# Performance work log

Measured on AMD Instinct MI355X. Metric: run time of the kernel, lower is better.

The kernel has to match this reference:

```python
import jax, jax.numpy as jnp
import numpy as np

MODEL_DIM = 1024
RANK = 128

def setup_inputs() -> dict:
    key = jax.random.key(0)
    k1, k2 = jax.random.split(key)
    batch = jax.random.normal(k1, (8, 512, MODEL_DIM), dtype=jnp.float32)
    # nn.init.uniform_(proj, -0.05, 0.05)
    proj = jax.random.uniform(k2, (MODEL_DIM, RANK), dtype=jnp.float32, minval=-0.05, maxval=0.05)
    return {"batch": batch, "proj": proj}

def reference(batch, proj):
    # project: (B, S, D) @ (D, R) -> (B, S, R)
    transformed = jnp.matmul(batch, proj)
    # all-pairs squared L2 distance via broadcast diff, matching the torch math
    # diffs: (B, S, S, R)
    diffs = transformed[:, :, None, :] - transformed[:, None, :, :]
    squared_distances = jnp.sum(diffs * diffs, axis=-1)  # (B, S, S)
    return squared_distances
```

## Files before the change

### kernel.cpp

```cpp
#include <hip/hip_runtime.h>

#define SEQ 512
#define MD  1024
#define RK  128

typedef __attribute__((ext_vector_type(8))) short  bf16x8;
typedef __attribute__((ext_vector_type(4))) float  floatx4;
typedef __attribute__((ext_vector_type(4))) unsigned int uint4v;
typedef __attribute__((ext_vector_type(4))) unsigned short ushortx4;

__device__ inline unsigned short f2bf(float f) {
    union { float f; unsigned u; } v; v.f = f;
    unsigned r = v.u + 0x7fffu + ((v.u >> 16) & 1u);
    return (unsigned short)(r >> 16);
}

__global__ __launch_bounds__(256) void transpose_proj(
    const float* __restrict__ proj, unsigned short* __restrict__ Pt)
{
    __shared__ float Ls[64 * 68];
    const int t  = threadIdx.x;
    const int k0 = (blockIdx.x >> 1) * 64;
    const int n0 = (blockIdx.x & 1) * 64;

    {
        int kr = t >> 2;
        int nc = (t & 3) * 16;
        #pragma unroll
        for (int c = 0; c < 4; ++c) {
            float4 v = *(const float4*)(proj + (size_t)(k0 + kr) * RK + n0 + nc + c * 4);
            *(float4*)(Ls + kr * 68 + nc + c * 4) = v;
        }
    }
    __syncthreads();
    {
        int nl = t >> 2;
        int kh = (t & 3) * 16;
        unsigned short tmp[16];
        #pragma unroll
        for (int kk = 0; kk < 16; ++kk)
            tmp[kk] = f2bf(Ls[(kh + kk) * 68 + nl]);
        *(uint4v*)(Pt + (size_t)(n0 + nl) * MD + k0 + kh)     = *(uint4v*)(tmp);
        *(uint4v*)(Pt + (size_t)(n0 + nl) * MD + k0 + kh + 8) = *(uint4v*)(tmp + 8);
    }
}

#define REDW 2112

__global__ __launch_bounds__(512) void proj_mfma(
    const float* __restrict__ batch, const unsigned short* __restrict__ Pt,
    unsigned short* __restrict__ T, float* __restrict__ Nrm)
{
    __shared__ float Red[8 * REDW];

    const int t    = threadIdx.x;
    const int w    = t >> 6;
    const int l    = t & 63;
    const int lm   = l & 15;
    const int quad = l >> 4;
    const int r0   = blockIdx.x * 16;

    floatx4 acc[8];
    #pragma unroll
    for (int i = 0; i < 8; ++i) acc[i] = (floatx4){0.f, 0.f, 0.f, 0.f};

    const float* arow = batch + (size_t)(r0 + lm) * MD + w * 128 + quad * 8;

    #pragma unroll
    for (int s = 0; s < 4; ++s) {
        float4 a0 = *(const float4*)(arow + s * 32);
        float4 a1 = *(const float4*)(arow + s * 32 + 4);
        bf16x8 av;
        av[0] = (short)f2bf(a0.x); av[1] = (short)f2bf(a0.y);
        av[2] = (short)f2bf(a0.z); av[3] = (short)f2bf(a0.w);
        av[4] = (short)f2bf(a1.x); av[5] = (short)f2bf(a1.y);
        av[6] = (short)f2bf(a1.z); av[7] = (short)f2bf(a1.w);
        #pragma unroll
        for (int nt = 0; nt < 8; ++nt) {
            bf16x8 bv = *(const bf16x8*)(Pt + (size_t)(nt * 16 + lm) * MD
                                         + w * 128 + s * 32 + quad * 8);
            acc[nt] = __builtin_amdgcn_mfma_f32_16x16x32_bf16(av, bv, acc[nt], 0, 0, 0);
        }
    }

    #pragma unroll
    for (int nt = 0; nt < 8; ++nt) {
        #pragma unroll
        for (int r = 0; r < 4; ++r) {
            Red[w * REDW + (quad * 4 + r) * 132 + nt * 16 + lm] = acc[nt][r];
        }
    }
    __syncthreads();

    {
        const int row  = t >> 5;
        const int col4 = (t & 31) * 4;
        float4 s4 = {0.f, 0.f, 0.f, 0.f};
        #pragma unroll
        for (int ww = 0; ww < 8; ++ww) {
            float4 p = *(const float4*)(Red + ww * REDW + row * 132 + col4);
            s4.x += p.x; s4.y += p.y; s4.z += p.z; s4.w += p.w;
        }
        unsigned short tmp[4];
        tmp[0] = f2bf(s4.x); tmp[1] = f2bf(s4.y);
        tmp[2] = f2bf(s4.z); tmp[3] = f2bf(s4.w);
        *(ushortx4*)(T + (size_t)(r0 + row) * RK + col4) = *(ushortx4*)tmp;

        float ss = s4.x * s4.x + s4.y * s4.y + s4.z * s4.z + s4.w * s4.w;
        ss += __shfl_xor(ss, 1,  64);
        ss += __shfl_xor(ss, 2,  64);
        ss += __shfl_xor(ss, 4,  64);
        ss += __shfl_xor(ss, 8,  64);
        ss += __shfl_xor(ss, 16, 64);
        if ((t & 31) == 0) Nrm[r0 + row] = ss;
    }
}

#define LDB 136

__global__ __launch_bounds__(256) void dist_mfma(
    const unsigned short* __restrict__ T, const float* __restrict__ Nrm,
    float* __restrict__ out)
{
    __shared__ unsigned short Ti[64 * LDB];
    __shared__ unsigned short Tj[64 * LDB];
    __shared__ float nI[64], nJ[64];

    const int t    = threadIdx.x;
    const int w    = t >> 6;
    const int l    = t & 63;
    const int lm   = l & 15;
    const int quad = l >> 4;
    const int jt = blockIdx.x, it = blockIdx.y, b = blockIdx.z;
    const int i0 = it * 64, j0 = jt * 64;
    const unsigned short* Tb = T + (size_t)b * SEQ * RK;

    {
        int row = t >> 2, kq = (t & 3) * 32;
        const unsigned short* si = Tb + (size_t)(i0 + row) * RK + kq;
        const unsigned short* sj = Tb + (size_t)(j0 + row) * RK + kq;
        #pragma unroll
        for (int q = 0; q < 4; ++q) {
            *(uint4v*)(Ti + row * LDB + kq + q * 8) = *(const uint4v*)(si + q * 8);
            *(uint4v*)(Tj + row * LDB + kq + q * 8) = *(const uint4v*)(sj + q * 8);
        }
        if (t < 64)                nI[t]      = Nrm[(size_t)b * SEQ + i0 + t];
        else if (t < 128)          nJ[t - 64] = Nrm[(size_t)b * SEQ + j0 + (t - 64)];
    }
    __syncthreads();

    floatx4 acc[4];
    #pragma unroll
    for (int i = 0; i < 4; ++i) acc[i] = (floatx4){0.f, 0.f, 0.f, 0.f};

    #pragma unroll
    for (int s = 0; s < 4; ++s) {
        bf16x8 av = *(const bf16x8*)(Ti + (w * 16 + lm) * LDB + s * 32 + quad * 8);
        #pragma unroll
        for (int nt = 0; nt < 4; ++nt) {
            bf16x8 bv = *(const bf16x8*)(Tj + (nt * 16 + lm) * LDB + s * 32 + quad * 8);
            acc[nt] = __builtin_amdgcn_mfma_f32_16x16x32_bf16(av, bv, acc[nt], 0, 0, 0);
        }
    }

    float niv[4];
    #pragma unroll
    for (int r = 0; r < 4; ++r) niv[r] = nI[w * 16 + quad * 4 + r];

    float* ob = out + ((size_t)b * SEQ + (i0 + w * 16)) * SEQ + j0;
    #pragma unroll
    for (int nt = 0; nt < 4; ++nt) {
        float njv = nJ[nt * 16 + lm];
        #pragma unroll
        for (int r = 0; r < 4; ++r) {
            ob[(size_t)(quad * 4 + r) * SEQ + nt * 16 + lm] =
                niv[r] + njv - 2.f * acc[nt][r];
        }
    }
}

extern "C" void kernel_launch(void* const* d_in, const int* in_sizes, int n_in,
                              void* d_out, int out_size, void* d_ws, size_t ws_size,
                              hipStream_t stream) {
    const float* batch = (const float*)d_in[0];
    const float* proj  = (const float*)d_in[1];
    float* out = (float*)d_out;

    unsigned short* T   = (unsigned short*)d_ws;
    unsigned short* Pt  = (unsigned short*)((char*)d_ws + (1 << 20));
    float*          Nrm = (float*)((char*)d_ws + (1 << 20) + (1 << 18));

    transpose_proj<<<32, 256, 0, stream>>>(proj, Pt);
    proj_mfma<<<256, 512, 0, stream>>>(batch, Pt, T, Nrm);
    dist_mfma<<<dim3(8, 8, 8), 256, 0, stream>>>(T, Nrm, out);
}
```

Baseline: 79.58 us.

## Fuse transpose, projection and distance kernels into one cooperative launch

Replaces three separate kernel launches with a single cooperative kernel of 512 blocks that uses grid-wide syncs between the proj-transpose, projection GEMM and pairwise-distance phases. The projection phase now uses 256-thread blocks with 4 waves each covering 256 of K, so the shared-memory reduction has 4 partials instead of 8. This is meant to remove inter-kernel launch gaps. In exchange it adds grid.sync overhead and fewer threads in the projection stage, and it depends on all 512 blocks being co-resident.

Result: slower. 210.5 us (+164.5%).

```diff
diff --git a/kernel.cpp b/kernel.cpp
--- a/kernel.cpp
+++ b/kernel.cpp
@@ -1,4 +1,7 @@
 #include <hip/hip_runtime.h>
+#include <hip/hip_cooperative_groups.h>
+
+namespace cg = cooperative_groups;
 
 #define SEQ 512
 #define MD  1024
@@ -15,166 +18,170 @@
     return (unsigned short)(r >> 16);
 }
 
-__global__ __launch_bounds__(256) void transpose_proj(
-    const float* __restrict__ proj, unsigned short* __restrict__ Pt)
+#define LDB  136
+#define REDW 2112
+
+__global__ __launch_bounds__(256, 2) void fused_probe(
+    const float* __restrict__ batch, const float* __restrict__ proj,
+    unsigned short* __restrict__ Pt, unsigned short* __restrict__ T,
+    float* __restrict__ Nrm, float* __restrict__ out)
 {
-    __shared__ float Ls[64 * 68];
-    const int t  = threadIdx.x;
-    const int k0 = (blockIdx.x >> 1) * 64;
-    const int n0 = (blockIdx.x & 1) * 64;
+    __shared__ float smem[8832];
+
+    const int t   = threadIdx.x;
+    const int bid = blockIdx.x;
+    cg::grid_group grid = cg::this_grid();
+
+    if (bid < 32) {
+        float* Ls = smem;
+        const int k0 = (bid >> 1) * 64;
+        const int n0 = (bid & 1) * 64;
+        {
+            int kr = t >> 2, nc = (t & 3) * 16;
+            #pragma unroll
+            for (int c = 0; c < 4; ++c) {
+                float4 v = *(const float4*)(proj + (size_t)(k0 + kr) * RK + n0 + nc + c * 4);
+                *(float4*)(Ls + kr * 68 + nc + c * 4) = v;
+            }
+        }
+        __syncthreads();
+        {
+            int nl = t >> 2, kh = (t & 3) * 16;
+            unsigned short tmp[16];
+            #pragma unroll
+            for (int kk = 0; kk < 16; ++kk)
+                tmp[kk] = f2bf(Ls[(kh + kk) * 68 + nl]);
+            *(uint4v*)(Pt + (size_t)(n0 + nl) * MD + k0 + kh)     = *(uint4v*)(tmp);
+            *(uint4v*)(Pt + (size_t)(n0 + nl) * MD + k0 + kh + 8) = *(uint4v*)(tmp + 8);
+        }
+        __threadfence();
+    }
+    grid.sync();
+
+    if (bid < 256) {
+        float* Red = smem;
+        const int w    = t >> 6;
+        const int l    = t & 63;
+        const int lm   = l & 15;
+        const int quad = l >> 4;
+        const int r0   = bid * 16;
+
+        floatx4 acc[8];
+        #pragma unroll
+        for (int i = 0; i < 8; ++i) acc[i] = (floatx4){0.f, 0.f, 0.f, 0.f};
+
+        const float*          arow = batch + (size_t)(r0 + lm) * MD + w * 256 + quad * 8;
+        const unsigned short* brow = Pt + (size_t)lm * MD + w * 256 + quad * 8;
+
+        #pragma unroll
+        for (int s = 0; s < 8; ++s) {
+            float4 a0 = *(const float4*)(arow + s * 32);
+            float4 a1 = *(const float4*)(arow + s * 32 + 4);
+            bf16x8 av;
+            av[0] = (short)f2bf(a0.x); av[1] = (short)f2bf(a0.y);
+            av[2] = (short)f2bf(a0.z); av[3] = (short)f2bf(a0.w);
+            av[4] = (short)f2bf(a1.x); av[5] = (short)f2bf(a1.y);
+            av[6] = (short)f2bf(a1.z); av[7] = (short)f2bf(a1.w);
+            #pragma unroll
+            for (int nt = 0; nt < 8; ++nt) {
+                bf16x8 bv = *(const bf16x8*)(brow + (size_t)nt * 16 * MD + s * 32);
+                acc[nt] = __builtin_amdgcn_mfma_f32_16x16x32_bf16(av, bv, acc[nt], 0, 0, 0);
+            }
+        }
+
+        #pragma unroll
+        for (int nt = 0; nt < 8; ++nt) {
+            #pragma unroll
+            for (int r = 0; r < 4; ++r)
+                Red[w * REDW + (quad * 4 + r) * 132 + nt * 16 + lm] = acc[nt][r];
+        }
+        __syncthreads();
+
+        {
+            const int row = t >> 4;
+            const int c8  = (t & 15) * 8;
+            float4 s0 = {0.f,0.f,0.f,0.f}, s1 = {0.f,0.f,0.f,0.f};
+            #pragma unroll
+            for (int ww = 0; ww < 4; ++ww) {
+                float4 p0 = *(const float4*)(Red + ww * REDW + row * 132 + c8);
+                float4 p1 = *(const float4*)(Red + ww * REDW + row * 132 + c8 + 4);
+                s0.x += p0.x; s0.y += p0.y; s0.z += p0.z; s0.w += p0.w;
+                s1.x += p1.x; s1.y += p1.y; s1.z += p1.z; s1.w += p1.w;
+            }
+            unsigned short tmp[8];
+            tmp[0] = f2bf(s0.x); tmp[1] = f2bf(s0.y); tmp[2] = f2bf(s0.z); tmp[3] = f2bf(s0.w);
+            tmp[4] = f2bf(s1.x); tmp[5] = f2bf(s1.y); tmp[6] = f2bf(s1.z); tmp[7] = f2bf(s1.w);
+            *(uint4v*)(T + (size_t)(r0 + row) * RK + c8) = *(uint4v*)tmp;
+
+            float ss = s0.x*s0.x + s0.y*s0.y + s0.z*s0.z + s0.w*s0.w
+                     + s1.x*s1.x + s1.y*s1.y + s1.z*s1.z + s1.w*s1.w;
+            ss += __shfl_xor(ss, 1, 64);
+            ss += __shfl_xor(ss, 2, 64);
+            ss += __shfl_xor(ss, 4, 64);
+            ss += __shfl_xor(ss, 8, 64);
+            if ((t & 15) == 0) Nrm[r0 + row] = ss;
+        }
+        __threadfence();
+    }
+    grid.sync();
 
     {
-        int kr = t >> 2;
-        int nc = (t & 3) * 16;
-        #pragma unroll
-        for (int c = 0; c < 4; ++c) {
-            float4 v = *(const float4*)(proj + (size_t)(k0 + kr) * RK + n0 + nc + c * 4);
-            *(float4*)(Ls + kr * 68 + nc + c * 4) = v;
-        }
-    }
-    __syncthreads();
-    {
-        int nl = t >> 2;
-        int kh = (t & 3) * 16;
-        unsigned short tmp[16];
-        #pragma unroll
-        for (int kk = 0; kk < 16; ++kk)
-            tmp[kk] = f2bf(Ls[(kh + kk) * 68 + nl]);
-        *(uint4v*)(Pt + (size_t)(n0 + nl) * MD + k0 + kh)     = *(uint4v*)(tmp);
-        *(uint4v*)(Pt + (size_t)(n0 + nl) * MD + k0 + kh + 8) = *(uint4v*)(tmp + 8);
-    }
-}
-
-#define REDW 2112
-
-__global__ __launch_bounds__(512) void proj_mfma(
-    const float* __restrict__ batch, const unsigned short* __restrict__ Pt,
-    unsigned short* __restrict__ T, float* __restrict__ Nrm)
-{
-    __shared__ float Red[8 * REDW];
-
-    const int t    = threadIdx.x;
-    const int w    = t >> 6;
-    const int l    = t & 63;
-    const int lm   = l & 15;
-    const int quad = l >> 4;
-    const int r0   = blockIdx.x * 16;
-
-    floatx4 acc[8];
-    #pragma unroll
-    for (int i = 0; i < 8; ++i) acc[i] = (floatx4){0.f, 0.f, 0.f, 0.f};
-
-    const float* arow = batch + (size_t)(r0 + lm) * MD + w * 128 + quad * 8;
-
-    #pragma unroll
-    for (int s = 0; s < 4; ++s) {
-        float4 a0 = *(const float4*)(arow + s * 32);
-        float4 a1 = *(const float4*)(arow + s * 32 + 4);
-        bf16x8 av;
-        av[0] = (short)f2bf(a0.x); av[1] = (short)f2bf(a0.y);
-        av[2] = (short)f2bf(a0.z); av[3] = (short)f2bf(a0.w);
-        av[4] = (short)f2bf(a1.x); av[5] = (short)f2bf(a1.y);
-        av[6] = (short)f2bf(a1.z); av[7] = (short)f2bf(a1.w);
-        #pragma unroll
-        for (int nt = 0; nt < 8; ++nt) {
-            bf16x8 bv = *(const bf16x8*)(Pt + (size_t)(nt * 16 + lm) * MD
-                                         + w * 128 + s * 32 + quad * 8);
-            acc[nt] = __builtin_amdgcn_mfma_f32_16x16x32_bf16(av, bv, acc[nt], 0, 0, 0);
-        }
-    }
-
-    #pragma unroll
-    for (int nt = 0; nt < 8; ++nt) {
-        #pragma unroll
-        for (int r = 0; r < 4; ++r) {
-            Red[w * REDW + (quad * 4 + r) * 132 + nt * 16 + lm] = acc[nt][r];
-        }
-    }
-    __syncthreads();
-
-    {
-        const int row  = t >> 5;
-        const int col4 = (t & 31) * 4;
-        float4 s4 = {0.f, 0.f, 0.f, 0.f};
-        #pragma unroll
-        for (int ww = 0; ww < 8; ++ww) {
-            float4 p = *(const float4*)(Red + ww * REDW + row * 132 + col4);
-            s4.x += p.x; s4.y += p.y; s4.z += p.z; s4.w += p.w;
-        }
-        unsigned short tmp[4];
-        tmp[0] = f2bf(s4.x); tmp[1] = f2bf(s4.y);
-        tmp[2] = f2bf(s4.z); tmp[3] = f2bf(s4.w);
-        *(ushortx4*)(T + (size_t)(r0 + row) * RK + col4) = *(ushortx4*)tmp;
-
-        float ss = s4.x * s4.x + s4.y * s4.y + s4.z * s4.z + s4.w * s4.w;
-        ss += __shfl_xor(ss, 1,  64);
-        ss += __shfl_xor(ss, 2,  64);
-        ss += __shfl_xor(ss, 4,  64);
-        ss += __shfl_xor(ss, 8,  64);
-        ss += __shfl_xor(ss, 16, 64);
-        if ((t & 31) == 0) Nrm[r0 + row] = ss;
-    }
-}
-
-#define LDB 136
-
-__global__ __launch_bounds__(256) void dist_mfma(
-    const unsigned short* __restrict__ T, const float* __restrict__ Nrm,
-    float* __restrict__ out)
-{
-    __shared__ unsigned short Ti[64 * LDB];
-    __shared__ unsigned short Tj[64 * LDB];
-    __shared__ float nI[64], nJ[64];
-
-    const int t    = threadIdx.x;
-    const int w    = t >> 6;
-    const int l    = t & 63;
-    const int lm   = l & 15;
-    const int quad = l >> 4;
-    const int jt = blockIdx.x, it = blockIdx.y, b = blockIdx.z;
-    const int i0 = it * 64, j0 = jt * 64;
-    const unsigned short* Tb = T + (size_t)b * SEQ * RK;
-
-    {
-        int row = t >> 2, kq = (t & 3) * 32;
-        const unsigned short* si = Tb + (size_t)(i0 + row) * RK + kq;
-        const unsigned short* sj = Tb + (size_t)(j0 + row) * RK + kq;
-        #pragma unroll
-        for (int q = 0; q < 4; ++q) {
-            *(uint4v*)(Ti + row * LDB + kq + q * 8) = *(const uint4v*)(si + q * 8);
-            *(uint4v*)(Tj + row * LDB + kq + q * 8) = *(const uint4v*)(sj + q * 8);
-        }
-        if (t < 64)                nI[t]      = Nrm[(size_t)b * SEQ + i0 + t];
-        else if (t < 128)          nJ[t - 64] = Nrm[(size_t)b * SEQ + j0 + (t - 64)];
-    }
-    __syncthreads();
-
-    floatx4 acc[4];
-    #pragma unroll
-    for (int i = 0; i < 4; ++i) acc[i] = (floatx4){0.f, 0.f, 0.f, 0.f};
-
-    #pragma unroll
-    for (int s = 0; s < 4; ++s) {
-        bf16x8 av = *(const bf16x8*)(Ti + (w * 16 + lm) * LDB + s * 32 + quad * 8);
+        unsigned short* Ti = (unsigned short*)smem;
+        unsigned short* Tj = Ti + 64 * LDB;
+        float* nI = (float*)(Tj + 64 * LDB);
+        float* nJ = nI + 64;
+
+        const int w    = t >> 6;
+        const int l    = t & 63;
+        const int lm   = l & 15;
+        const int quad = l >> 4;
+        const int b  = bid >> 6;
+        const int it = (bid >> 3) & 7;
+        const int jt = bid & 7;
+        const int i0 = it * 64, j0 = jt * 64;
+        const unsigned short* Tb = T + (size_t)b * SEQ * RK;
+
+        {
+            int row = t >> 2, kq = (t & 3) * 32;
+            const unsigned short* si = Tb + (size_t)(i0 + row) * RK + kq;
+            const unsigned short* sj = Tb + (size_t)(j0 + row) * RK + kq;
+            #pragma unroll
+            for (int q = 0; q < 4; ++q) {
+                *(uint4v*)(Ti + row * LDB + kq + q * 8) = *(const uint4v*)(si + q * 8);
+                *(uint4v*)(Tj + row * LDB + kq + q * 8) = *(const uint4v*)(sj + q * 8);
+            }
+            if (t < 64)       nI[t]      = Nrm[(size_t)b * SEQ + i0 + t];
+            else if (t < 128) nJ[t - 64] = Nrm[(size_t)b * SEQ + j0 + (t - 64)];
+        }
+        __syncthreads();
+
+        floatx4 acc[4];
+        #pragma unroll
+        for (int i = 0; i < 4; ++i) acc[i] = (floatx4){0.f, 0.f, 0.f, 0.f};
+
+        #pragma unroll
+        for (int s = 0; s < 4; ++s) {
+            bf16x8 av = *(const bf16x8*)(Ti + (w * 16 + lm) * LDB + s * 32 + quad * 8);
+            #pragma unroll
+            for (int nt = 0; nt < 4; ++nt) {
+                bf16x8 bv = *(const bf16x8*)(Tj + (nt * 16 + lm) * LDB + s * 32 + quad * 8);
+                acc[nt] = __builtin_amdgcn_mfma_f32_16x16x32_bf16(av, bv, acc[nt], 0, 0, 0);
+            }
+        }
+
+        float niv[4];
+        #pragma unroll
+        for (int r = 0; r < 4; ++r) niv[r] = nI[w * 16 + quad * 4 + r];
+
+        float* ob = out + ((size_t)b * SEQ + (i0 + w * 16)) * SEQ + j0;
         #pragma unroll
         for (int nt = 0; nt < 4; ++nt) {
-            bf16x8 bv = *(const bf16x8*)(Tj + (nt * 16 + lm) * LDB + s * 32 + quad * 8);
-            acc[nt] = __builtin_amdgcn_mfma_f32_16x16x32_bf16(av, bv, acc[nt], 0, 0, 0);
-        }
-    }
-
-    float niv[4];
-    #pragma unroll
-    for (int r = 0; r < 4; ++r) niv[r] = nI[w * 16 + quad * 4 + r];
-
-    float* ob = out + ((size_t)b * SEQ + (i0 + w * 16)) * SEQ + j0;
-    #pragma unroll
-    for (int nt = 0; nt < 4; ++nt) {
-        float njv = nJ[nt * 16 + lm];
-        #pragma unroll
-        for (int r = 0; r < 4; ++r) {
-            ob[(size_t)(quad * 4 + r) * SEQ + nt * 16 + lm] =
-                niv[r] + njv - 2.f * acc[nt][r];
+            float njv = nJ[nt * 16 + lm];
+            #pragma unroll
+            for (int r = 0; r < 4; ++r) {
+                ob[(size_t)(quad * 4 + r) * SEQ + nt * 16 + lm] =
+                    niv[r] + njv - 2.f * acc[nt][r];
+            }
         }
     }
 }
@@ -190,7 +197,8 @@
     unsigned short* Pt  = (unsigned short*)((char*)d_ws + (1 << 20));
     float*          Nrm = (float*)((char*)d_ws + (1 << 20) + (1 << 18));
 
-    transpose_proj<<<32, 256, 0, stream>>>(proj, Pt);
-    proj_mfma<<<256, 512, 0, stream>>>(batch, Pt, T, Nrm);
-    dist_mfma<<<dim3(8, 8, 8), 256, 0, stream>>>(T, Nrm, out);
+    void* args[] = { (void*)&batch, (void*)&proj, (void*)&Pt, (void*)&T,
+                     (void*)&Nrm, (void*)&out };
+    hipLaunchCooperativeKernel((const void*)fused_probe, dim3(512), dim3(256),
+                               args, 0, stream);
 }
```
